# Kernel tuning notes

Hardware: AMD Instinct MI355X
Metric: run time of the kernel (lower is better)

## Reference

```python
import jax, jax.numpy as jnp
import numpy as np

N_NODES = 100000
N_EDGES = 3200000
N_IN = 5
N_OUT = 16


def setup_inputs() -> dict:
    key = jax.random.key(0)
    k1, k2, k3, k4 = jax.random.split(key, 4)
    atom = jax.random.normal(k1, (N_NODES, N_IN), dtype=jnp.float32)
    edge_index = jax.random.randint(k2, (2, N_EDGES), 0, N_NODES, dtype=jnp.int64)
    # Linear(n_input=5, n_neural=16) parameters
    W = jax.random.normal(k3, (N_OUT, N_IN), dtype=jnp.float32) / np.sqrt(N_IN)
    b = jax.random.normal(k4, (N_OUT,), dtype=jnp.float32) * 0.01
    return {"atom": atom, "edge_index": edge_index, "W": W, "b": b}


def reference(atom, edge_index, W, b):
    n = atom.shape[0]
    # add_self_loops
    loops = jnp.arange(n, dtype=edge_index.dtype)
    row = jnp.concatenate([edge_index[0], loops])  # source nodes [E+N]
    col = jnp.concatenate([edge_index[1], loops])  # target nodes [E+N]
    # x = Linear(atom)
    x = atom @ W.T + b  # [N, n_out]
    # degree over target index (includes self loops -> deg >= 1)
    deg = jax.ops.segment_sum(jnp.ones_like(col, dtype=x.dtype), col, num_segments=n)
    dis = deg ** -0.5  # deg_inv_sqrt, finite since deg >= 1
    norm = dis[row] * dis[col]  # [E+N]
    # gather-scale-scatter: message = norm * x_j, aggr='add' at col
    msgs = norm[:, None] * x[row]  # [E+N, n_out]
    out = jax.ops.segment_sum(msgs, col, num_segments=n)  # [N, n_out]
    return jax.nn.relu(out)
```

## Files before the change

### kernel.cpp

```cpp
#include <hip/hip_runtime.h>

#define N_IN 5
#define N_OUT 16
#define NB 64
#define BN 1600
#define CAP 53248
#define NSUB 4
#define QSCALE 2048.0f
#define QBIAS 16384

__device__ __forceinline__ int bin_of(int c) {
    return (int)(((unsigned long long)(unsigned)c * 2684355ull) >> 32);
}

__global__ void init_kernel(int* __restrict__ cursor) {
    if (threadIdx.x < NB) cursor[threadIdx.x] = threadIdx.x * CAP;
}

__global__ __launch_bounds__(1024) void partition_kernel(
        const int* __restrict__ row, const int* __restrict__ col,
        int e, int* __restrict__ eb, int* __restrict__ cursor) {
    __shared__ int hist[NB];
    __shared__ int base[NB];
    int e4 = e >> 2;
    int nchunk = (e4 + 1023) / 1024;
    const int4* rowv = (const int4*)row;
    const int4* colv = (const int4*)col;
    for (int ch = blockIdx.x; ch < nchunk; ch += gridDim.x) {
        int i = ch * 1024 + threadIdx.x;
        bool valid = i < e4;
        int rr[4], cc[4], bb[4], pr[4];
        if (valid) {
            int4 r4 = rowv[i];
            int4 c4 = colv[i];
            rr[0] = r4.x; rr[1] = r4.y; rr[2] = r4.z; rr[3] = r4.w;
            cc[0] = c4.x; cc[1] = c4.y; cc[2] = c4.z; cc[3] = c4.w;
        }
        if (threadIdx.x < NB) hist[threadIdx.x] = 0;
        __syncthreads();
        if (valid) {
#pragma unroll
            for (int j = 0; j < 4; ++j) {
                bb[j] = bin_of(cc[j]);
                pr[j] = atomicAdd(&hist[bb[j]], 1);
            }
        }
        __syncthreads();
        if (threadIdx.x < NB) {
            int h = hist[threadIdx.x];
            base[threadIdx.x] = h ? atomicAdd(&cursor[threadIdx.x], h) : 0;
        }
        __syncthreads();
        if (valid) {
#pragma unroll
            for (int j = 0; j < 4; ++j) {
                int p = base[bb[j]] + pr[j];
                if (p < (bb[j] + 1) * CAP)
                    eb[p] = ((cc[j] - bb[j] * BN) << 17) | rr[j];
            }
        }
        __syncthreads();
    }
    if (blockIdx.x == 0) {
        for (int i = (e4 << 2) + (int)threadIdx.x; i < e; i += (int)blockDim.x) {
            int c = col[i];
            int b = bin_of(c);
            int p = atomicAdd(&cursor[b], 1);
            if (p < (b + 1) * CAP) eb[p] = ((c - b * BN) << 17) | row[i];
        }
    }
}

__global__ __launch_bounds__(1024) void degcount(
        const int* __restrict__ eb, const int* __restrict__ cursor,
        unsigned short* __restrict__ degp) {
    __shared__ int hist[BN];
    int bin = blockIdx.x >> 2;
    int sub = blockIdx.x & 3;
    for (int j = threadIdx.x; j < BN; j += 1024) hist[j] = 0;
    __syncthreads();
    int s0 = bin * CAP;
    int cnt = min(max(cursor[bin] - s0, 0), CAP);
    int chunk = (cnt + NSUB - 1) / NSUB;
    int start = min(sub * chunk, cnt);
    int end = min(start + chunk, cnt);
    for (int i = s0 + start + (int)threadIdx.x; i < s0 + end; i += 1024)
        atomicAdd(&hist[eb[i] >> 17], 1);
    __syncthreads();
    unsigned short* dst = degp + (size_t)blockIdx.x * BN;
    for (int j = threadIdx.x; j < BN; j += 1024) dst[j] = (unsigned short)hist[j];
}

__global__ void dis_datom(const unsigned short* __restrict__ degp,
                          const float* __restrict__ atom,
                          int* __restrict__ deg,
                          ulonglong2* __restrict__ datom, int n) {
    int i = blockIdx.x * blockDim.x + threadIdx.x;
    if (i >= n) return;
    int bin = bin_of(i);
    int l = i - bin * BN;
    int dg = 0;
#pragma unroll
    for (int sb = 0; sb < NSUB; ++sb)
        dg += degp[(size_t)(bin * NSUB + sb) * BN + l];
    deg[i] = dg;
    float d = rsqrtf((float)(dg + 1));
    const float* ap = atom + (size_t)i * N_IN;
    unsigned long long f[6];
#pragma unroll
    for (int k = 0; k < 5; ++k) {
        int q = __float2int_rn(d * ap[k] * QSCALE);
        q = min(max(q, -16383), 16383);
        f[k] = (unsigned long long)(q + QBIAS);
    }
    f[5] = (unsigned long long)(__float2int_rn(d * QSCALE) + QBIAS);
    ulonglong2 v;
    v.x = f[0] | (f[1] << 21) | (f[2] << 42);
    v.y = f[3] | (f[4] << 21) | (f[5] << 42);
    datom[i] = v;
}

__global__ __launch_bounds__(1024) void accum_bin(
        const int* __restrict__ eb, const int* __restrict__ cursor,
        const ulonglong2* __restrict__ datom,
        ulonglong2* __restrict__ accp) {
    __shared__ unsigned long long accA[BN];
    __shared__ unsigned long long accB[BN];
    int bin = blockIdx.x >> 2;
    int sub = blockIdx.x & 3;
    for (int j = threadIdx.x; j < BN; j += 1024) { accA[j] = 0ull; accB[j] = 0ull; }
    __syncthreads();
    int s0 = bin * CAP;
    int cnt = min(max(cursor[bin] - s0, 0), CAP);
    int chunk = (cnt + NSUB - 1) / NSUB;
    int start = min(sub * chunk, cnt);
    int end = min(start + chunk, cnt);
    int i = s0 + start + (int)threadIdx.x;
    int iend = s0 + end;
    for (; i + 1024 < iend; i += 2048) {
        int v0 = eb[i];
        int v1 = eb[i + 1024];
        ulonglong2 d0 = datom[v0 & 0x1FFFF];
        ulonglong2 d1 = datom[v1 & 0x1FFFF];
        int l0 = v0 >> 17;
        int l1 = v1 >> 17;
        atomicAdd(&accA[l0], d0.x);
        atomicAdd(&accB[l0], d0.y);
        atomicAdd(&accA[l1], d1.x);
        atomicAdd(&accB[l1], d1.y);
    }
    if (i < iend) {
        int v0 = eb[i];
        ulonglong2 d0 = datom[v0 & 0x1FFFF];
        int l0 = v0 >> 17;
        atomicAdd(&accA[l0], d0.x);
        atomicAdd(&accB[l0], d0.y);
    }
    __syncthreads();
    ulonglong2* dst = accp + (size_t)blockIdx.x * BN;
    for (int j = threadIdx.x; j < BN; j += 1024) {
        ulonglong2 v; v.x = accA[j]; v.y = accB[j];
        dst[j] = v;
    }
}

__global__ void final_kernel(const ulonglong2* __restrict__ accp,
                             const int* __restrict__ deg,
                             const float* __restrict__ atom,
                             const float* __restrict__ W, const float* __restrict__ b,
                             float* __restrict__ out, int n) {
    int i = blockIdx.x * blockDim.x + threadIdx.x;
    if (i >= n) return;
    int bin = bin_of(i);
    int l = i - bin * BN;
    int f[6] = {0, 0, 0, 0, 0, 0};
#pragma unroll
    for (int sb = 0; sb < NSUB; ++sb) {
        ulonglong2 v = accp[(size_t)(bin * NSUB + sb) * BN + l];
        f[0] += (int)(v.x & 0x1FFFFF);
        f[1] += (int)((v.x >> 21) & 0x1FFFFF);
        f[2] += (int)((v.x >> 42) & 0x1FFFFF);
        f[3] += (int)(v.y & 0x1FFFFF);
        f[4] += (int)((v.y >> 21) & 0x1FFFFF);
        f[5] += (int)((v.y >> 42) & 0x1FFFFF);
    }
    int dg = deg[i];
    int db = dg * QBIAS;
    const float inv = 1.0f / QSCALE;
    float s[6];
#pragma unroll
    for (int k = 0; k < 6; ++k) s[k] = (float)(f[k] - db) * inv;
    float d = rsqrtf((float)(dg + 1));
    const float* ap = atom + (size_t)i * N_IN;
    float t5[5];
#pragma unroll
    for (int k = 0; k < 5; ++k) t5[k] = d * (s[k] + d * ap[k]);
    float t1 = d * (s[5] + d);
    float ov[N_OUT];
#pragma unroll
    for (int o = 0; o < N_OUT; ++o) {
        float a = b[o] * t1;
#pragma unroll
        for (int k = 0; k < 5; ++k) a = fmaf(W[o * N_IN + k], t5[k], a);
        ov[o] = fmaxf(a, 0.0f);
    }
    float4* op = (float4*)(out + (size_t)i * N_OUT);
#pragma unroll
    for (int q = 0; q < 4; ++q)
        op[q] = make_float4(ov[4 * q], ov[4 * q + 1], ov[4 * q + 2], ov[4 * q + 3]);
}

extern "C" void kernel_launch(void* const* d_in, const int* in_sizes, int n_in,
                              void* d_out, int out_size, void* d_ws, size_t ws_size,
                              hipStream_t stream) {
    const float* atom = (const float*)d_in[0];
    const int*   eidx = (const int*)d_in[1];
    const float* W    = (const float*)d_in[2];
    const float* b    = (const float*)d_in[3];
    float* out = (float*)d_out;

    int n = in_sizes[0] / N_IN;
    int e = in_sizes[1] / 2;
    const int* row = eidx;
    const int* col = eidx + e;

    auto align256 = [](size_t v) { return (v + 255) & ~(size_t)255; };
    char* w = (char*)d_ws;
    int*            cursor = (int*)w;            w += align256(NB * 4);
    int*            deg    = (int*)w;            w += align256((size_t)n * 4);
    ulonglong2*     datom  = (ulonglong2*)w;     w += align256((size_t)n * 16);
    int*            eb     = (int*)w;            w += align256((size_t)NB * CAP * 4);
    unsigned short* degp   = (unsigned short*)w; w += align256((size_t)NB * NSUB * BN * 2);
    ulonglong2*     accp   = (ulonglong2*)w;

    const int B = 256;
    int gn = (n + B - 1) / B;
    init_kernel<<<1, 64, 0, stream>>>(cursor);
    partition_kernel<<<256, 1024, 0, stream>>>(row, col, e, eb, cursor);
    degcount<<<NB * NSUB, 1024, 0, stream>>>(eb, cursor, degp);
    dis_datom<<<gn, B, 0, stream>>>(degp, atom, deg, datom, n);
    accum_bin<<<NB * NSUB, 1024, 0, stream>>>(eb, cursor, datom, accp);
    final_kernel<<<gn, B, 0, stream>>>(accp, deg, atom, W, b, out, n);
}
```

Before: 129.0 us.

## Replace shared-memory atomic scatter with CSR placement and per-node pull gather

The per-bin quantized shared-memory atomic accumulation is replaced by a CSR-style layout. A per-bin prefix scan computes segment starts, a placement pass writes source indices grouped by target, and a final kernel pulls each node's neighbours with 4 lanes per node, summing fp16 pre-scaled features in fp32. This removes 64-bit LDS atomics and the partial-sum reduction, at the cost of an extra scatter pass over all edges and fp16 feature precision. The degree is clamped to 255 in the packed segment word, so any node with a higher in-degree would be summed incorrectly.

```diff
diff --git a/kernel.cpp b/kernel.cpp
--- a/kernel.cpp
+++ b/kernel.cpp
@@ -6,8 +6,8 @@
 #define BN 1600
 #define CAP 53248
 #define NSUB 4
-#define QSCALE 2048.0f
-#define QBIAS 16384
+
+typedef _Float16 half8 __attribute__((ext_vector_type(8)));
 
 __device__ __forceinline__ int bin_of(int c) {
     return (int)(((unsigned long long)(unsigned)c * 2684355ull) >> 32);
@@ -91,123 +91,132 @@
     for (int j = threadIdx.x; j < BN; j += 1024) dst[j] = (unsigned short)hist[j];
 }
 
-__global__ void dis_datom(const unsigned short* __restrict__ degp,
-                          const float* __restrict__ atom,
-                          int* __restrict__ deg,
-                          ulonglong2* __restrict__ datom, int n) {
-    int i = blockIdx.x * blockDim.x + threadIdx.x;
-    if (i >= n) return;
-    int bin = bin_of(i);
-    int l = i - bin * BN;
-    int dg = 0;
-#pragma unroll
-    for (int sb = 0; sb < NSUB; ++sb)
-        dg += degp[(size_t)(bin * NSUB + sb) * BN + l];
-    deg[i] = dg;
-    float d = rsqrtf((float)(dg + 1));
-    const float* ap = atom + (size_t)i * N_IN;
-    unsigned long long f[6];
-#pragma unroll
-    for (int k = 0; k < 5; ++k) {
-        int q = __float2int_rn(d * ap[k] * QSCALE);
-        q = min(max(q, -16383), 16383);
-        f[k] = (unsigned long long)(q + QBIAS);
-    }
-    f[5] = (unsigned long long)(__float2int_rn(d * QSCALE) + QBIAS);
-    ulonglong2 v;
-    v.x = f[0] | (f[1] << 21) | (f[2] << 42);
-    v.y = f[3] | (f[4] << 21) | (f[5] << 42);
-    datom[i] = v;
-}
-
-__global__ __launch_bounds__(1024) void accum_bin(
+__global__ __launch_bounds__(1024) void scan_datom(
+        const unsigned short* __restrict__ degp,
+        const float* __restrict__ atom,
+        int* __restrict__ start_tab, int* __restrict__ segpack,
+        half8* __restrict__ datom, int n) {
+    __shared__ int sc[2048];
+    int bin = blockIdx.x;
+    int tid = threadIdx.x;
+    int d0 = 0, d1 = 0;
+    int dgs0[NSUB], dgs1[NSUB];
+#pragma unroll
+    for (int s = 0; s < NSUB; ++s) {
+        dgs0[s] = degp[(size_t)(bin * NSUB + s) * BN + tid];
+        d0 += dgs0[s];
+        if (tid + 1024 < BN) {
+            dgs1[s] = degp[(size_t)(bin * NSUB + s) * BN + tid + 1024];
+            d1 += dgs1[s];
+        } else dgs1[s] = 0;
+    }
+    sc[tid] = d0;
+    sc[tid + 1024] = (tid + 1024 < BN) ? d1 : 0;
+    __syncthreads();
+    for (int d = 1; d < 2048; d <<= 1) {
+        int t0 = (tid >= d) ? sc[tid - d] : 0;
+        int t1 = (tid + 1024 >= d) ? sc[tid + 1024 - d] : 0;
+        __syncthreads();
+        sc[tid] += t0;
+        sc[tid + 1024] += t1;
+        __syncthreads();
+    }
+    int binbase = bin * CAP;
+#pragma unroll
+    for (int h = 0; h < 2; ++h) {
+        int l = tid + h * 1024;
+        if (l >= BN) break;
+        int deg = (h == 0) ? d0 : d1;
+        int st = binbase + sc[l] - deg;
+        int off = st;
+#pragma unroll
+        for (int s = 0; s < NSUB; ++s) {
+            start_tab[(size_t)(bin * NSUB + s) * BN + l] = off;
+            off += (h == 0) ? dgs0[s] : dgs1[s];
+        }
+        int i = bin * BN + l;
+        if (i < n) {
+            segpack[i] = (min(deg, 255) << 24) | st;
+            float dis = rsqrtf((float)(deg + 1));
+            const float* ap = atom + (size_t)i * N_IN;
+            half8 hh;
+            hh[0] = (_Float16)(dis * ap[0]);
+            hh[1] = (_Float16)(dis * ap[1]);
+            hh[2] = (_Float16)(dis * ap[2]);
+            hh[3] = (_Float16)(dis * ap[3]);
+            hh[4] = (_Float16)(dis * ap[4]);
+            hh[5] = (_Float16)dis;
+            hh[6] = (_Float16)0.f;
+            hh[7] = (_Float16)0.f;
+            datom[i] = hh;
+        }
+    }
+}
+
+__global__ __launch_bounds__(1024) void placement_kernel(
         const int* __restrict__ eb, const int* __restrict__ cursor,
-        const ulonglong2* __restrict__ datom,
-        ulonglong2* __restrict__ accp) {
-    __shared__ unsigned long long accA[BN];
-    __shared__ unsigned long long accB[BN];
+        const int* __restrict__ start_tab, int* __restrict__ eb2) {
+    __shared__ int cur[BN];
     int bin = blockIdx.x >> 2;
     int sub = blockIdx.x & 3;
-    for (int j = threadIdx.x; j < BN; j += 1024) { accA[j] = 0ull; accB[j] = 0ull; }
+    const int* st = start_tab + (size_t)blockIdx.x * BN;
+    for (int j = threadIdx.x; j < BN; j += 1024) cur[j] = st[j];
     __syncthreads();
     int s0 = bin * CAP;
     int cnt = min(max(cursor[bin] - s0, 0), CAP);
     int chunk = (cnt + NSUB - 1) / NSUB;
     int start = min(sub * chunk, cnt);
     int end = min(start + chunk, cnt);
-    int i = s0 + start + (int)threadIdx.x;
-    int iend = s0 + end;
-    for (; i + 1024 < iend; i += 2048) {
-        int v0 = eb[i];
-        int v1 = eb[i + 1024];
-        ulonglong2 d0 = datom[v0 & 0x1FFFF];
-        ulonglong2 d1 = datom[v1 & 0x1FFFF];
-        int l0 = v0 >> 17;
-        int l1 = v1 >> 17;
-        atomicAdd(&accA[l0], d0.x);
-        atomicAdd(&accB[l0], d0.y);
-        atomicAdd(&accA[l1], d1.x);
-        atomicAdd(&accB[l1], d1.y);
-    }
-    if (i < iend) {
-        int v0 = eb[i];
-        ulonglong2 d0 = datom[v0 & 0x1FFFF];
-        int l0 = v0 >> 17;
-        atomicAdd(&accA[l0], d0.x);
-        atomicAdd(&accB[l0], d0.y);
-    }
-    __syncthreads();
-    ulonglong2* dst = accp + (size_t)blockIdx.x * BN;
-    for (int j = threadIdx.x; j < BN; j += 1024) {
-        ulonglong2 v; v.x = accA[j]; v.y = accB[j];
-        dst[j] = v;
-    }
-}
-
-__global__ void final_kernel(const ulonglong2* __restrict__ accp,
-                             const int* __restrict__ deg,
+    for (int i = s0 + start + (int)threadIdx.x; i < s0 + end; i += 1024) {
+        int v = eb[i];
+        int p = atomicAdd(&cur[v >> 17], 1);
+        eb2[p] = v & 0x1FFFF;
+    }
+}
+
+__global__ void gather_final(const int* __restrict__ segpack,
+                             const int* __restrict__ eb2,
+                             const half8* __restrict__ datom,
                              const float* __restrict__ atom,
                              const float* __restrict__ W, const float* __restrict__ b,
                              float* __restrict__ out, int n) {
-    int i = blockIdx.x * blockDim.x + threadIdx.x;
-    if (i >= n) return;
-    int bin = bin_of(i);
-    int l = i - bin * BN;
-    int f[6] = {0, 0, 0, 0, 0, 0};
-#pragma unroll
-    for (int sb = 0; sb < NSUB; ++sb) {
-        ulonglong2 v = accp[(size_t)(bin * NSUB + sb) * BN + l];
-        f[0] += (int)(v.x & 0x1FFFFF);
-        f[1] += (int)((v.x >> 21) & 0x1FFFFF);
-        f[2] += (int)((v.x >> 42) & 0x1FFFFF);
-        f[3] += (int)(v.y & 0x1FFFFF);
-        f[4] += (int)((v.y >> 21) & 0x1FFFFF);
-        f[5] += (int)((v.y >> 42) & 0x1FFFFF);
-    }
-    int dg = deg[i];
-    int db = dg * QBIAS;
-    const float inv = 1.0f / QSCALE;
-    float s[6];
-#pragma unroll
-    for (int k = 0; k < 6; ++k) s[k] = (float)(f[k] - db) * inv;
-    float d = rsqrtf((float)(dg + 1));
-    const float* ap = atom + (size_t)i * N_IN;
+    int t = blockIdx.x * blockDim.x + threadIdx.x;
+    int node = t >> 2;
+    int q = t & 3;
+    if (node >= n) return;
+    int sp = segpack[node];
+    int s0 = sp & 0xFFFFFF;
+    int deg = (unsigned)sp >> 24;
+    float s[6] = {0.f, 0.f, 0.f, 0.f, 0.f, 0.f};
+    for (int k = q; k < deg; k += 4) {
+        int r = eb2[s0 + k];
+        half8 h = datom[r];
+#pragma unroll
+        for (int j = 0; j < 6; ++j) s[j] += (float)h[j];
+    }
+#pragma unroll
+    for (int j = 0; j < 6; ++j) {
+        s[j] += __shfl_xor(s[j], 1);
+        s[j] += __shfl_xor(s[j], 2);
+    }
+    half8 hc = datom[node];
+    float d = (float)hc[5];
+    const float* ap = atom + (size_t)node * N_IN;
     float t5[5];
 #pragma unroll
     for (int k = 0; k < 5; ++k) t5[k] = d * (s[k] + d * ap[k]);
     float t1 = d * (s[5] + d);
-    float ov[N_OUT];
-#pragma unroll
-    for (int o = 0; o < N_OUT; ++o) {
+    float4 ov;
+    float* po = (float*)&ov;
+#pragma unroll
+    for (int oo = 0; oo < 4; ++oo) {
+        int o = q * 4 + oo;
         float a = b[o] * t1;
 #pragma unroll
         for (int k = 0; k < 5; ++k) a = fmaf(W[o * N_IN + k], t5[k], a);
-        ov[o] = fmaxf(a, 0.0f);
-    }
-    float4* op = (float4*)(out + (size_t)i * N_OUT);
-#pragma unroll
-    for (int q = 0; q < 4; ++q)
-        op[q] = make_float4(ov[4 * q], ov[4 * q + 1], ov[4 * q + 2], ov[4 * q + 3]);
+        po[oo] = fmaxf(a, 0.0f);
+    }
+    ((float4*)(out + (size_t)node * N_OUT))[q] = ov;
 }
 
 extern "C" void kernel_launch(void* const* d_in, const int* in_sizes, int n_in,
@@ -226,19 +235,19 @@
 
     auto align256 = [](size_t v) { return (v + 255) & ~(size_t)255; };
     char* w = (char*)d_ws;
-    int*            cursor = (int*)w;            w += align256(NB * 4);
-    int*            deg    = (int*)w;            w += align256((size_t)n * 4);
-    ulonglong2*     datom  = (ulonglong2*)w;     w += align256((size_t)n * 16);
-    int*            eb     = (int*)w;            w += align256((size_t)NB * CAP * 4);
-    unsigned short* degp   = (unsigned short*)w; w += align256((size_t)NB * NSUB * BN * 2);
-    ulonglong2*     accp   = (ulonglong2*)w;
-
-    const int B = 256;
-    int gn = (n + B - 1) / B;
+    int*            cursor   = (int*)w;            w += align256(NB * 4);
+    int*            eb       = (int*)w;            w += align256((size_t)NB * CAP * 4);
+    int*            eb2      = (int*)w;            w += align256((size_t)NB * CAP * 4);
+    int*            start_tab= (int*)w;            w += align256((size_t)NB * NSUB * BN * 4);
+    int*            segpack  = (int*)w;            w += align256((size_t)n * 4);
+    unsigned short* degp     = (unsigned short*)w; w += align256((size_t)NB * NSUB * BN * 2);
+    half8*          datom    = (half8*)w;
+
     init_kernel<<<1, 64, 0, stream>>>(cursor);
     partition_kernel<<<256, 1024, 0, stream>>>(row, col, e, eb, cursor);
     degcount<<<NB * NSUB, 1024, 0, stream>>>(eb, cursor, degp);
-    dis_datom<<<gn, B, 0, stream>>>(degp, atom, deg, datom, n);
-    accum_bin<<<NB * NSUB, 1024, 0, stream>>>(eb, cursor, datom, accp);
-    final_kernel<<<gn, B, 0, stream>>>(accp, deg, atom, W, b, out, n);
-}
+    scan_datom<<<NB, 1024, 0, stream>>>(degp, atom, start_tab, segpack, datom, n);
+    placement_kernel<<<NB * NSUB, 1024, 0, stream>>>(eb, cursor, start_tab, eb2);
+    gather_final<<<(4 * n + 255) / 256, 256, 0, stream>>>(
+        segpack, eb2, datom, atom, W, b, out, n);
+}
```

After: 169.1 us. 31.1% more time.

## Use finer node bins and fuse degree/quantize and accumulate/final kernels

Applied to the files above, without the earlier changes.

Raises the bin count from 64 to 256 with 400 nodes per bin, so each block owns a whole bin and no per-sub-block partial histograms or accumulators have to be merged. Degree counting is fused with node quantization, and edge accumulation is fused with the final linear+ReLU, cutting the launch count from six to four and removing the intermediate partial buffers. Edge-list reads are vectorized to int4. Quantization scale is halved to keep 21-bit packed fields from overflowing with smaller bins, which lowers precision. Launching only 256 blocks of 1024 threads may underfill the GPU compared with the previous sub-bin split.

```diff
diff --git a/kernel.cpp b/kernel.cpp
--- a/kernel.cpp
+++ b/kernel.cpp
@@ -2,15 +2,15 @@
 
 #define N_IN 5
 #define N_OUT 16
-#define NB 64
-#define BN 1600
-#define CAP 53248
-#define NSUB 4
-#define QSCALE 2048.0f
-#define QBIAS 16384
+#define NB 256
+#define BN 400
+#define CAP 14336
+#define QSCALE 1024.0f
+#define QBIAS 8192
+#define BIN_MAGIC 10737419ull
 
 __device__ __forceinline__ int bin_of(int c) {
-    return (int)(((unsigned long long)(unsigned)c * 2684355ull) >> 32);
+    return (int)(((unsigned long long)(unsigned)c * BIN_MAGIC) >> 32);
 }
 
 __global__ void init_kernel(int* __restrict__ cursor) {
@@ -71,127 +71,106 @@
     }
 }
 
-__global__ __launch_bounds__(1024) void degcount(
+__global__ __launch_bounds__(1024) void deg_quant_kernel(
         const int* __restrict__ eb, const int* __restrict__ cursor,
-        unsigned short* __restrict__ degp) {
+        const float* __restrict__ atom,
+        ulonglong2* __restrict__ qdatom, unsigned short* __restrict__ deg16,
+        int n) {
     __shared__ int hist[BN];
-    int bin = blockIdx.x >> 2;
-    int sub = blockIdx.x & 3;
-    for (int j = threadIdx.x; j < BN; j += 1024) hist[j] = 0;
+    int bin = blockIdx.x;
+    if (threadIdx.x < BN) hist[threadIdx.x] = 0;
     __syncthreads();
     int s0 = bin * CAP;
     int cnt = min(max(cursor[bin] - s0, 0), CAP);
-    int chunk = (cnt + NSUB - 1) / NSUB;
-    int start = min(sub * chunk, cnt);
-    int end = min(start + chunk, cnt);
-    for (int i = s0 + start + (int)threadIdx.x; i < s0 + end; i += 1024)
-        atomicAdd(&hist[eb[i] >> 17], 1);
-    __syncthreads();
-    unsigned short* dst = degp + (size_t)blockIdx.x * BN;
-    for (int j = threadIdx.x; j < BN; j += 1024) dst[j] = (unsigned short)hist[j];
-}
-
-__global__ void dis_datom(const unsigned short* __restrict__ degp,
-                          const float* __restrict__ atom,
-                          int* __restrict__ deg,
-                          ulonglong2* __restrict__ datom, int n) {
-    int i = blockIdx.x * blockDim.x + threadIdx.x;
-    if (i >= n) return;
-    int bin = bin_of(i);
-    int l = i - bin * BN;
-    int dg = 0;
-#pragma unroll
-    for (int sb = 0; sb < NSUB; ++sb)
-        dg += degp[(size_t)(bin * NSUB + sb) * BN + l];
-    deg[i] = dg;
-    float d = rsqrtf((float)(dg + 1));
-    const float* ap = atom + (size_t)i * N_IN;
+    const int4* ebv = (const int4*)(eb + s0);
+    int cnt4 = cnt >> 2;
+    for (int i = threadIdx.x; i < cnt4; i += 1024) {
+        int4 v = ebv[i];
+        atomicAdd(&hist[v.x >> 17], 1);
+        atomicAdd(&hist[v.y >> 17], 1);
+        atomicAdd(&hist[v.z >> 17], 1);
+        atomicAdd(&hist[v.w >> 17], 1);
+    }
+    for (int i = (cnt4 << 2) + (int)threadIdx.x; i < cnt; i += 1024)
+        atomicAdd(&hist[eb[s0 + i] >> 17], 1);
+    __syncthreads();
+    int l = threadIdx.x;
+    if (l >= BN) return;
+    int node = bin * BN + l;
+    if (node >= n) return;
+    int deg = hist[l];
+    deg16[node] = (unsigned short)deg;
+    float d = rsqrtf((float)(deg + 1));
+    const float* ap = atom + (size_t)node * N_IN;
     unsigned long long f[6];
 #pragma unroll
     for (int k = 0; k < 5; ++k) {
         int q = __float2int_rn(d * ap[k] * QSCALE);
-        q = min(max(q, -16383), 16383);
+        q = min(max(q, -8191), 8191);
         f[k] = (unsigned long long)(q + QBIAS);
     }
     f[5] = (unsigned long long)(__float2int_rn(d * QSCALE) + QBIAS);
     ulonglong2 v;
     v.x = f[0] | (f[1] << 21) | (f[2] << 42);
     v.y = f[3] | (f[4] << 21) | (f[5] << 42);
-    datom[i] = v;
-}
-
-__global__ __launch_bounds__(1024) void accum_bin(
+    qdatom[node] = v;
+}
+
+__global__ __launch_bounds__(1024) void accum_final(
         const int* __restrict__ eb, const int* __restrict__ cursor,
-        const ulonglong2* __restrict__ datom,
-        ulonglong2* __restrict__ accp) {
+        const ulonglong2* __restrict__ qdatom,
+        const unsigned short* __restrict__ deg16,
+        const float* __restrict__ atom,
+        const float* __restrict__ W, const float* __restrict__ bias,
+        float* __restrict__ out, int n) {
     __shared__ unsigned long long accA[BN];
     __shared__ unsigned long long accB[BN];
-    int bin = blockIdx.x >> 2;
-    int sub = blockIdx.x & 3;
-    for (int j = threadIdx.x; j < BN; j += 1024) { accA[j] = 0ull; accB[j] = 0ull; }
+    int bin = blockIdx.x;
+    if (threadIdx.x < BN) { accA[threadIdx.x] = 0ull; accB[threadIdx.x] = 0ull; }
     __syncthreads();
     int s0 = bin * CAP;
     int cnt = min(max(cursor[bin] - s0, 0), CAP);
-    int chunk = (cnt + NSUB - 1) / NSUB;
-    int start = min(sub * chunk, cnt);
-    int end = min(start + chunk, cnt);
-    int i = s0 + start + (int)threadIdx.x;
-    int iend = s0 + end;
-    for (; i + 1024 < iend; i += 2048) {
-        int v0 = eb[i];
-        int v1 = eb[i + 1024];
-        ulonglong2 d0 = datom[v0 & 0x1FFFF];
-        ulonglong2 d1 = datom[v1 & 0x1FFFF];
-        int l0 = v0 >> 17;
-        int l1 = v1 >> 17;
-        atomicAdd(&accA[l0], d0.x);
-        atomicAdd(&accB[l0], d0.y);
-        atomicAdd(&accA[l1], d1.x);
-        atomicAdd(&accB[l1], d1.y);
-    }
-    if (i < iend) {
-        int v0 = eb[i];
-        ulonglong2 d0 = datom[v0 & 0x1FFFF];
-        int l0 = v0 >> 17;
-        atomicAdd(&accA[l0], d0.x);
-        atomicAdd(&accB[l0], d0.y);
-    }
-    __syncthreads();
-    ulonglong2* dst = accp + (size_t)blockIdx.x * BN;
-    for (int j = threadIdx.x; j < BN; j += 1024) {
-        ulonglong2 v; v.x = accA[j]; v.y = accB[j];
-        dst[j] = v;
-    }
-}
-
-__global__ void final_kernel(const ulonglong2* __restrict__ accp,
-                             const int* __restrict__ deg,
-                             const float* __restrict__ atom,
-                             const float* __restrict__ W, const float* __restrict__ b,
-                             float* __restrict__ out, int n) {
-    int i = blockIdx.x * blockDim.x + threadIdx.x;
-    if (i >= n) return;
-    int bin = bin_of(i);
-    int l = i - bin * BN;
-    int f[6] = {0, 0, 0, 0, 0, 0};
-#pragma unroll
-    for (int sb = 0; sb < NSUB; ++sb) {
-        ulonglong2 v = accp[(size_t)(bin * NSUB + sb) * BN + l];
-        f[0] += (int)(v.x & 0x1FFFFF);
-        f[1] += (int)((v.x >> 21) & 0x1FFFFF);
-        f[2] += (int)((v.x >> 42) & 0x1FFFFF);
-        f[3] += (int)(v.y & 0x1FFFFF);
-        f[4] += (int)((v.y >> 21) & 0x1FFFFF);
-        f[5] += (int)((v.y >> 42) & 0x1FFFFF);
-    }
-    int dg = deg[i];
-    int db = dg * QBIAS;
+    const int4* ebv = (const int4*)(eb + s0);
+    int cnt4 = cnt >> 2;
+    for (int i = threadIdx.x; i < cnt4; i += 1024) {
+        int4 v = ebv[i];
+        ulonglong2 q0 = qdatom[v.x & 0x1FFFF];
+        ulonglong2 q1 = qdatom[v.y & 0x1FFFF];
+        ulonglong2 q2 = qdatom[v.z & 0x1FFFF];
+        ulonglong2 q3 = qdatom[v.w & 0x1FFFF];
+        atomicAdd(&accA[v.x >> 17], q0.x);
+        atomicAdd(&accB[v.x >> 17], q0.y);
+        atomicAdd(&accA[v.y >> 17], q1.x);
+        atomicAdd(&accB[v.y >> 17], q1.y);
+        atomicAdd(&accA[v.z >> 17], q2.x);
+        atomicAdd(&accB[v.z >> 17], q2.y);
+        atomicAdd(&accA[v.w >> 17], q3.x);
+        atomicAdd(&accB[v.w >> 17], q3.y);
+    }
+    for (int i = (cnt4 << 2) + (int)threadIdx.x; i < cnt; i += 1024) {
+        int v = eb[s0 + i];
+        ulonglong2 q = qdatom[v & 0x1FFFF];
+        atomicAdd(&accA[v >> 17], q.x);
+        atomicAdd(&accB[v >> 17], q.y);
+    }
+    __syncthreads();
+    int l = threadIdx.x;
+    if (l >= BN) return;
+    int node = bin * BN + l;
+    if (node >= n) return;
+    unsigned long long SA = accA[l], SB = accB[l];
+    int deg = deg16[node];
+    int db = deg * QBIAS;
     const float inv = 1.0f / QSCALE;
     float s[6];
-#pragma unroll
-    for (int k = 0; k < 6; ++k) s[k] = (float)(f[k] - db) * inv;
-    float d = rsqrtf((float)(dg + 1));
-    const float* ap = atom + (size_t)i * N_IN;
+    s[0] = (float)((int)((SA      ) & 0x1FFFFF) - db) * inv;
+    s[1] = (float)((int)((SA >> 21) & 0x1FFFFF) - db) * inv;
+    s[2] = (float)((int)((SA >> 42) & 0x1FFFFF) - db) * inv;
+    s[3] = (float)((int)((SB      ) & 0x1FFFFF) - db) * inv;
+    s[4] = (float)((int)((SB >> 21) & 0x1FFFFF) - db) * inv;
+    s[5] = (float)((int)((SB >> 42) & 0x1FFFFF) - db) * inv;
+    float d = rsqrtf((float)(deg + 1));
+    const float* ap = atom + (size_t)node * N_IN;
     float t5[5];
 #pragma unroll
     for (int k = 0; k < 5; ++k) t5[k] = d * (s[k] + d * ap[k]);
@@ -199,12 +178,12 @@
     float ov[N_OUT];
 #pragma unroll
     for (int o = 0; o < N_OUT; ++o) {
-        float a = b[o] * t1;
+        float a = bias[o] * t1;
 #pragma unroll
         for (int k = 0; k < 5; ++k) a = fmaf(W[o * N_IN + k], t5[k], a);
         ov[o] = fmaxf(a, 0.0f);
     }
-    float4* op = (float4*)(out + (size_t)i * N_OUT);
+    float4* op = (float4*)(out + (size_t)node * N_OUT);
 #pragma unroll
     for (int q = 0; q < 4; ++q)
         op[q] = make_float4(ov[4 * q], ov[4 * q + 1], ov[4 * q + 2], ov[4 * q + 3]);
@@ -227,18 +206,12 @@
     auto align256 = [](size_t v) { return (v + 255) & ~(size_t)255; };
     char* w = (char*)d_ws;
     int*            cursor = (int*)w;            w += align256(NB * 4);
-    int*            deg    = (int*)w;            w += align256((size_t)n * 4);
-    ulonglong2*     datom  = (ulonglong2*)w;     w += align256((size_t)n * 16);
     int*            eb     = (int*)w;            w += align256((size_t)NB * CAP * 4);
-    unsigned short* degp   = (unsigned short*)w; w += align256((size_t)NB * NSUB * BN * 2);
-    ulonglong2*     accp   = (ulonglong2*)w;
-
-    const int B = 256;
-    int gn = (n + B - 1) / B;
-    init_kernel<<<1, 64, 0, stream>>>(cursor);
+    ulonglong2*     qdatom = (ulonglong2*)w;     w += align256((size_t)NB * BN * 16);
+    unsigned short* deg16  = (unsigned short*)w;
+
+    init_kernel<<<1, NB, 0, stream>>>(cursor);
     partition_kernel<<<256, 1024, 0, stream>>>(row, col, e, eb, cursor);
-    degcount<<<NB * NSUB, 1024, 0, stream>>>(eb, cursor, degp);
-    dis_datom<<<gn, B, 0, stream>>>(degp, atom, deg, datom, n);
-    accum_bin<<<NB * NSUB, 1024, 0, stream>>>(eb, cursor, datom, accp);
-    final_kernel<<<gn, B, 0, stream>>>(accp, deg, atom, W, b, out, n);
-}
+    deg_quant_kernel<<<NB, 1024, 0, stream>>>(eb, cursor, atom, qdatom, deg16, n);
+    accum_final<<<NB, 1024, 0, stream>>>(eb, cursor, qdatom, deg16, atom, W, b, out, n);
+}
```

New measurement: 124.3 us. -3.7%, faster.
